# Performance work log

Hardware: AMD Instinct MI355X
Metric: run time of the kernel (lower is better)

## Reference

```python
import jax, jax.numpy as jnp
import numpy as np

TEMPERATURE = 0.07
EPS = 1e-20

B, C, T, N = 16, 128, 8, 1024


def setup_inputs() -> dict:
    key = jax.random.key(0)
    feats = jax.random.normal(key, (B, C, T, N), dtype=jnp.float32)
    return {"feats": feats}


def reference(feats):
    # feats: [B, C, T, N] node features (post encoder+head).
    # L2-normalize along channel dim (FCHead normalizes embeddings in CRW).
    f = feats / (jnp.linalg.norm(feats, axis=1, keepdims=True) + 1e-12)

    # calc_affinity: pairwise affinity between consecutive frames -> [B, T-1, N, N]
    A = jnp.einsum("bctn,bctm->btnm", f[:, :, :-1], f[:, :, 1:])

    # calc_markov: temperature softmax over last dim (edge dropout off / eval)
    right = jax.nn.softmax(A / TEMPERATURE, axis=-1)                  # forward edges
    left = jax.nn.softmax(A.swapaxes(-1, -2) / TEMPERATURE, axis=-1)  # backward edges

    t_len = feats.shape[2]
    losses = []
    for i in range(1, t_len - 1):
        # palindrome walk: right[0..i] then left[i..0], chained BxNxN matmuls
        path = right[:, 0]
        for t in range(1, i + 1):
            path = path @ right[:, t]
        for t in range(i, -1, -1):
            path = path @ left[:, t]
        # cross_entropy(log(path+EPS), arange(N)) averaged over B*N rows
        logp = jax.nn.log_softmax(jnp.log(path + EPS), axis=-1)  # [B, N, N]
        diag = jnp.diagonal(logp, axis1=-2, axis2=-1)            # [B, N]
        losses.append(-jnp.mean(diag))
    return jnp.mean(jnp.stack(losses))
```

## Files before the change

kernel.cpp:

```cpp
#include <hip/hip_runtime.h>

typedef __attribute__((ext_vector_type(4))) float f32x4;
typedef __attribute__((ext_vector_type(8))) short bf16x8;
typedef __attribute__((ext_vector_type(8))) unsigned short ushort8;

#define NB 16
#define NC 128
#define NT 8
#define NN 1024
#define INV_T (1.0f/0.07f)
#define LDW 40

__device__ __forceinline__ unsigned short f2bf(float x){
  union { float f; unsigned int u; } v; v.f = x;
  unsigned int r = v.u + 0x7fffu + ((v.u >> 16) & 1u);
  return (unsigned short)(r >> 16);
}

__device__ __forceinline__ unsigned char f2fp8_sw(float x){
  if(!(x >= 9.765625e-4f)) return 0;
  if(x >= 448.f) return 0x7E;
  union { float f; unsigned int u; } v; v.f = x;
  int e = (int)((v.u >> 23) & 255) - 127;
  if(e >= -6){
    unsigned int m = v.u & 0x7FFFFFu;
    unsigned int r = m + 0x7FFFFu + ((m >> 20) & 1u);
    if(r & 0x800000u){ e++; r = 0; }
    unsigned int b = ((unsigned)(e + 7) << 3) | ((r >> 20) & 7u);
    if(b >= 0x7Fu) b = 0x7Eu;
    return (unsigned char)b;
  } else {
    float t = x * 512.f;
    int q = (int)(t + 0.5f);
    return (unsigned char)q;
  }
}

__device__ __forceinline__ unsigned int pk2fp8(float a, float b){
#if __has_builtin(__builtin_amdgcn_cvt_pk_fp8_f32)
  return (unsigned int)__builtin_amdgcn_cvt_pk_fp8_f32(a, b, 0, false);
#else
  return (unsigned int)f2fp8_sw(a) | ((unsigned int)f2fp8_sw(b) << 8);
#endif
}

__device__ __forceinline__ void gload16(const void* g, void* l){
  __builtin_amdgcn_global_load_lds((const __attribute__((address_space(1))) unsigned int*)g,
                                   (__attribute__((address_space(3))) unsigned int*)l,
                                   16, 0, 0);
}

__global__ void k_norm(const float* __restrict__ feats, unsigned short* __restrict__ fbuf){
  int n = blockIdx.x * 256 + threadIdx.x;
  int b = blockIdx.y >> 3, t = blockIdx.y & 7;
  const float* src = feats + (((size_t)b * NC) * NT + t) * NN + n;
  float ss = 0.f;
  #pragma unroll 8
  for(int c = 0; c < NC; c++){ float v = src[(size_t)c * NT * NN]; ss += v * v; }
  float sc = 1.f / (sqrtf(ss) + 1e-12f);
  unsigned short* dst = fbuf + (((size_t)b * NT + t) * NN + n) * NC;
  #pragma unroll 8
  for(int c = 0; c < NC; c++){ float v = src[(size_t)c * NT * NN]; dst[c] = f2bf(v * sc); }
}

__device__ __forceinline__ void stage_s(const unsigned short* __restrict__ g, int ldg, unsigned short* lds){
  int tid = threadIdx.x;
  #pragma unroll
  for(int j = 0; j < 2; j++){
    int chunk = tid + j * 256;
    int row = chunk >> 2, kc = chunk & 3;
    *(ushort8*)(lds + row * LDW + kc * 8) = *(const ushort8*)(g + (size_t)row * ldg + kc * 8);
  }
}

__device__ __forceinline__ bf16x8 frag_s(const unsigned short* lds, int r0, int lane){
  return *(const bf16x8*)(lds + (r0 + (lane & 15)) * LDW + (lane >> 4) * 8);
}

template<int MODE>
__global__ void gemm_small(const unsigned short* __restrict__ fbuf,
                           unsigned char* __restrict__ G,
                           float* __restrict__ rb, float* __restrict__ cb,
                           unsigned char* __restrict__ P0, unsigned char* __restrict__ M0,
                           int tsel)
{
  __shared__ __align__(16) unsigned short lA[128*LDW];
  __shared__ __align__(16) unsigned short lB[128*LDW];
  int b, t, brow, bcol;
  if(MODE == 0){
    int lin = blockIdx.x, x8 = lin & 7, q = lin >> 3;
    int blk = q & 63, g = (q >> 6) * 8 + x8;
    b = g / 7; t = g % 7;
    brow = (blk >> 3) << 7; bcol = (blk & 7) << 7;
  } else if(MODE == 2){
    int lin = blockIdx.x, x8 = lin & 7, q = lin >> 3;
    int blk = q & 63;
    b = (q >> 6) * 8 + x8; t = 0;
    brow = (blk >> 3) << 7; bcol = (blk & 7) << 7;
  } else {
    b = blockIdx.z; t = tsel;
    brow = blockIdx.x * 128; bcol = blockIdx.y * 128;
  }
  int tA = (MODE==2) ? 0 : t+1;
  int tB = (MODE==2) ? 1 : t;
  const unsigned short* Ab = fbuf + ((size_t)(b*NT+tA)*NN + brow) * NC;
  const unsigned short* Bb = fbuf + ((size_t)(b*NT+tB)*NN + bcol) * NC;
  int tid = threadIdx.x, lane = tid & 63, w = tid >> 6, wr = w >> 1, wc = w & 1;
  f32x4 acc[4][4];
  #pragma unroll
  for(int m=0;m<4;m++)
    #pragma unroll
    for(int n=0;n<4;n++) acc[m][n] = (f32x4){0.f,0.f,0.f,0.f};

  for(int kk=0; kk<4; kk++){
    __syncthreads();
    stage_s(Ab + kk*32, NC, lA);
    stage_s(Bb + kk*32, NC, lB);
    __syncthreads();
    bf16x8 fa[4], fg[4];
    #pragma unroll
    for(int x=0;x<4;x++){ fa[x] = frag_s(lA, wr*64+x*16, lane); fg[x] = frag_s(lB, wc*64+x*16, lane); }
    #pragma unroll
    for(int m=0;m<4;m++)
      #pragma unroll
      for(int n=0;n<4;n++)
        acc[m][n] = __builtin_amdgcn_mfma_f32_16x16x32_bf16(fa[m], fg[n], acc[m][n], 0, 0, 0);
  }

  float e[4][4][4];
  #pragma unroll
  for(int m=0;m<4;m++)
    #pragma unroll
    for(int n=0;n<4;n++)
      #pragma unroll
      for(int j=0;j<4;j++) e[m][n][j] = __expf(acc[m][n][j] * INV_T);

  if(MODE == 0){
    float* cbt = cb + ((size_t)b*7 + t) * NN;
    float* rbt = rb + ((size_t)b*7 + t) * NN;
    #pragma unroll
    for(int m=0;m<4;m++)
      #pragma unroll
      for(int j=0;j<4;j++){
        float s = e[m][0][j]+e[m][1][j]+e[m][2][j]+e[m][3][j];
        s += __shfl_xor(s,1); s += __shfl_xor(s,2); s += __shfl_xor(s,4); s += __shfl_xor(s,8);
        if((lane & 15) == 0){
          int row = brow + wr*64 + m*16 + (lane>>4)*4 + j;
          atomicAdd(&cbt[row], s);
        }
      }
    #pragma unroll
    for(int n=0;n<4;n++){
      float s = 0.f;
      #pragma unroll
      for(int m=0;m<4;m++)
        #pragma unroll
        for(int j=0;j<4;j++) s += e[m][n][j];
      s += __shfl_xor(s,16); s += __shfl_xor(s,32);
      if((lane >> 4) == 0){
        int col = bcol + wc*64 + n*16 + lane;
        atomicAdd(&rbt[col], s);
      }
    }
    if(G && t >= 1){
      unsigned char* Gt = G + ((size_t)(t-1)*NB + b) * ((size_t)NN*NN);
      #pragma unroll
      for(int m=0;m<4;m++)
        #pragma unroll
        for(int j=0;j<4;j++){
          int row = brow + wr*64 + m*16 + (lane>>4)*4 + j;
          unsigned char* gr = Gt + (size_t)row * NN + bcol + wc*64 + (lane&15);
          unsigned int p01 = pk2fp8(e[m][0][j]*0.0625f, e[m][1][j]*0.0625f);
          unsigned int p23 = pk2fp8(e[m][2][j]*0.0625f, e[m][3][j]*0.0625f);
          gr[0]  = (unsigned char)p01;
          gr[16] = (unsigned char)(p01 >> 8);
          gr[32] = (unsigned char)p23;
          gr[48] = (unsigned char)(p23 >> 8);
        }
    }
  } else if(MODE == 1){
    unsigned char* Gt = G + ((size_t)b << 20);
    #pragma unroll
    for(int m=0;m<4;m++)
      #pragma unroll
      for(int j=0;j<4;j++){
        int row = brow + wr*64 + m*16 + (lane>>4)*4 + j;
        unsigned char* gr = Gt + (size_t)row * NN + bcol + wc*64 + (lane&15);
        unsigned int p01 = pk2fp8(e[m][0][j]*0.0625f, e[m][1][j]*0.0625f);
        unsigned int p23 = pk2fp8(e[m][2][j]*0.0625f, e[m][3][j]*0.0625f);
        gr[0]  = (unsigned char)p01;
        gr[16] = (unsigned char)(p01 >> 8);
        gr[32] = (unsigned char)p23;
        gr[48] = (unsigned char)(p23 >> 8);
      }
  } else {
    const float* r0 = rb + (size_t)b*7*NN;
    const float* r1 = r0 + NN;
    const float* c0 = cb + (size_t)b*7*NN;
    unsigned char* Pt = P0 + ((size_t)b << 20);
    unsigned char* Mt = M0 + ((size_t)b << 20);
    float r1i[4], c0i[4];
    #pragma unroll
    for(int n=0;n<4;n++){
      int col = bcol + wc*64 + n*16 + (lane&15);
      r1i[n] = 65536.f / r1[col];
      c0i[n] = 1024.f / c0[col];
    }
    #pragma unroll
    for(int m=0;m<4;m++)
      #pragma unroll
      for(int j=0;j<4;j++){
        int row = brow + wr*64 + m*16 + (lane>>4)*4 + j;
        float r0i = 1.f / r0[row];
        unsigned char* pr = Pt + (size_t)row * NN + bcol + wc*64 + (lane&15);
        unsigned char* mr = Mt + (size_t)row * NN + bcol + wc*64 + (lane&15);
        unsigned int a01 = pk2fp8(e[m][0][j]*r0i*r1i[0], e[m][1][j]*r0i*r1i[1]);
        unsigned int a23 = pk2fp8(e[m][2][j]*r0i*r1i[2], e[m][3][j]*r0i*r1i[3]);
        unsigned int b01 = pk2fp8(e[m][0][j]*c0i[0], e[m][1][j]*c0i[1]);
        unsigned int b23 = pk2fp8(e[m][2][j]*c0i[2], e[m][3][j]*c0i[3]);
        pr[0]  = (unsigned char)a01;  pr[16] = (unsigned char)(a01 >> 8);
        pr[32] = (unsigned char)a23;  pr[48] = (unsigned char)(a23 >> 8);
        mr[0]  = (unsigned char)b01;  mr[16] = (unsigned char)(b01 >> 8);
        mr[32] = (unsigned char)b23;  mr[48] = (unsigned char)(b23 >> 8);
      }
  }
}

template<int LAST>
__global__ void __launch_bounds__(512, 2)
k_chain(const unsigned char* __restrict__ P, const unsigned char* __restrict__ M,
        const unsigned char* __restrict__ G,
        unsigned char* __restrict__ Pn, unsigned char* __restrict__ Mn,
        const float* __restrict__ rb, const float* __restrict__ cb,
        float* __restrict__ diag, int i)
{
  __shared__ __align__(16) unsigned char lP0[128*64], lM0[128*64], lG0[256*64];
  __shared__ __align__(16) unsigned char lP1[128*64], lM1[128*64], lG1[256*64];
  int lin = blockIdx.x, x8 = lin & 7, q = lin >> 3;
  int jj = q & 15, g = (q >> 4) * 8 + x8;
  int b = g >> 1, cbp = g & 1;
  int rowb = jj >> 1, cbk = cbp * 2 + (jj & 1);
  size_t mb = (size_t)b << 20;
  int brow = rowb * 128, bcol = cbk * 256;
  const unsigned char* Pb = P + mb + (size_t)brow * NN;
  const unsigned char* Mb = M + mb + (size_t)brow * NN;
  const unsigned char* Gb = G + mb + (size_t)bcol * NN;
  int tid = threadIdx.x, lane = tid & 63, w = tid >> 6, wr = w >> 2, wc = w & 3;
  int l15 = lane & 15, g4 = lane >> 4, sm = l15 & 6;

  int srow = tid >> 2;
  int gOff = (((tid & 3) ^ ((srow >> 1) & 3)) << 4);
  int so0 = ((g4 ^ sm) << 3);

  f32x4 aP[4][4], aM[4][4];
  #pragma unroll
  for(int m=0;m<4;m++)
    #pragma unroll
    for(int n=0;n<4;n++){ aP[m][n] = (f32x4){0.f,0.f,0.f,0.f}; aM[m][n] = (f32x4){0.f,0.f,0.f,0.f}; }

  auto stage = [&](int kk, unsigned char* lp, unsigned char* lm, unsigned char* lg){
    const unsigned char* ps = Pb + kk*64 + gOff;
    const unsigned char* ms = Mb + kk*64 + gOff;
    const unsigned char* gs = Gb + kk*64 + gOff;
    gload16(ps + (size_t)srow*NN,       lp + tid*16);
    gload16(ms + (size_t)srow*NN,       lm + tid*16);
    gload16(gs + (size_t)srow*NN,       lg + tid*16);
    gload16(gs + (size_t)(srow+128)*NN, lg + 8192 + tid*16);
  };

  auto compute = [&](const unsigned char* lp, const unsigned char* lm, const unsigned char* lg){
    #pragma unroll
    for(int kh = 0; kh < 2; kh++){
      int so = so0 ^ (kh << 5);
      long fP[4], fM[4], fG[4];
      #pragma unroll
      for(int x=0;x<4;x++){
        fP[x] = *(const long*)(lp + (wr*64 + x*16 + l15)*64 + so);
        fM[x] = *(const long*)(lm + (wr*64 + x*16 + l15)*64 + so);
        fG[x] = *(const long*)(lg + (wc*64 + x*16 + l15)*64 + so);
      }
      #pragma unroll
      for(int m=0;m<4;m++)
        #pragma unroll
        for(int n=0;n<4;n++){
          aP[m][n] = __builtin_amdgcn_mfma_f32_16x16x32_fp8_fp8(fP[m], fG[n], aP[m][n], 0, 0, 0);
          aM[m][n] = __builtin_amdgcn_mfma_f32_16x16x32_fp8_fp8(fM[m], fG[n], aM[m][n], 0, 0, 0);
        }
    }
  };

  stage(0, lP0, lM0, lG0);
  __syncthreads();
  #pragma unroll 1
  for(int kk = 0; kk < 16; kk += 2){
    if(kk + 1 < 16) stage(kk+1, lP1, lM1, lG1);
    compute(lP0, lM0, lG0);
    __syncthreads();
    if(kk + 2 < 16) stage(kk+2, lP0, lM0, lG0);
    compute(lP1, lM1, lG1);
    __syncthreads();
  }

  const float* ccur = cb + ((size_t)b*7 + i) * NN;
  const float* rnxt = rb + ((size_t)b*7 + i + 1) * NN;
  float cid[4], ciw[4], ri[4];
  #pragma unroll
  for(int n=0;n<4;n++){
    int col = bcol + wc*64 + n*16 + l15;
    float c1 = 1.f / ccur[col];
    cid[n] = c1;
    ciw[n] = 16.f * c1;
    ri[n]  = LAST ? 0.f : 16.f / rnxt[col];
  }
  float* dg = diag + ((size_t)b*6 + (i-1)) * NN;
  #pragma unroll
  for(int m=0;m<4;m++)
    #pragma unroll
    for(int j4=0;j4<4;j4++){
      int rowi = brow + wr*64 + m*16 + (lane>>4)*4 + j4;
      float s = 0.f;
      #pragma unroll
      for(int n=0;n<4;n++)
        s += aP[m][n][j4] * aM[m][n][j4] * cid[n];
      if(!LAST){
        unsigned char* pr = Pn + mb + (size_t)rowi * NN + bcol + wc*64 + l15;
        unsigned char* mr = Mn + mb + (size_t)rowi * NN + bcol + wc*64 + l15;
        unsigned int a01 = pk2fp8(aP[m][0][j4]*ri[0], aP[m][1][j4]*ri[1]);
        unsigned int a23 = pk2fp8(aP[m][2][j4]*ri[2], aP[m][3][j4]*ri[3]);
        unsigned int b01 = pk2fp8(aM[m][0][j4]*ciw[0], aM[m][1][j4]*ciw[1]);
        unsigned int b23 = pk2fp8(aM[m][2][j4]*ciw[2], aM[m][3][j4]*ciw[3]);
        pr[0]  = (unsigned char)a01;  pr[16] = (unsigned char)(a01 >> 8);
        pr[32] = (unsigned char)a23;  pr[48] = (unsigned char)(a23 >> 8);
        mr[0]  = (unsigned char)b01;  mr[16] = (unsigned char)(b01 >> 8);
        mr[32] = (unsigned char)b23;  mr[48] = (unsigned char)(b23 >> 8);
      }
      s += __shfl_xor(s,1); s += __shfl_xor(s,2); s += __shfl_xor(s,4); s += __shfl_xor(s,8);
      if((lane&15)==0) atomicAdd(&dg[rowi], s * (1.f/262144.f));
    }
}

__global__ void k_loss(const float* __restrict__ diag, float* __restrict__ out){
  __shared__ float red[16];
  float s = 0.f;
  for(int idx = threadIdx.x; idx < NB*6*NN; idx += 1024) s += __logf(diag[idx] + 1e-20f);
  s += __shfl_xor(s,1); s += __shfl_xor(s,2); s += __shfl_xor(s,4);
  s += __shfl_xor(s,8); s += __shfl_xor(s,16); s += __shfl_xor(s,32);
  if((threadIdx.x & 63) == 0) red[threadIdx.x >> 6] = s;
  __syncthreads();
  if(threadIdx.x == 0){
    float t = 0.f;
    for(int k = 0; k < 16; k++) t += red[k];
    out[0] = -t / (6.0f * NB * NN);
  }
}

__global__ void k_fail(float* out){ out[0] = 1.0e9f; }

extern "C" void kernel_launch(void* const* d_in, const int* in_sizes, int n_in,
                              void* d_out, int out_size, void* d_ws, size_t ws_size,
                              hipStream_t stream) {
  const float* feats = (const float*)d_in[0];
  float* out = (float*)d_out;
  char* ws = (char*)d_ws;
  size_t off = 0;
  auto alloc = [&](size_t bytes) -> char* {
    char* p = ws + off; off += (bytes + 255) & ~(size_t)255; return p;
  };
  const size_t plane = (size_t)NB * NN * NN;
  unsigned short* fb = (unsigned short*)alloc((size_t)NB*NT*NN*NC*2);
  unsigned char* Pa   = (unsigned char*)alloc(plane);
  unsigned char* Pbuf = (unsigned char*)alloc(plane);
  unsigned char* Ma   = (unsigned char*)alloc(plane);
  unsigned char* Mbuf = (unsigned char*)alloc(plane);
  float* rb = (float*)alloc((size_t)NB*7*NN*4);
  float* cb = (float*)alloc((size_t)NB*7*NN*4);
  float* dg = (float*)alloc((size_t)NB*6*NN*4);
  if(off + plane > ws_size){ k_fail<<<1,1,0,stream>>>(out); return; }
  bool big = (off + 6*plane) <= ws_size;
  unsigned char* G = (unsigned char*)alloc(big ? 6*plane : plane);

  hipMemsetAsync(rb, 0, (size_t)NB*7*NN*4 + (size_t)NB*7*NN*4 + (size_t)NB*6*NN*4, stream);

  k_norm<<<dim3(4, NB*NT), 256, 0, stream>>>(feats, fb);
  gemm_small<0><<<dim3(7168), 256, 0, stream>>>(fb, big ? G : nullptr, rb, cb, nullptr, nullptr, 0);
  gemm_small<2><<<dim3(1024), 256, 0, stream>>>(fb, nullptr, rb, cb, Pa, Ma, 0);

  unsigned char *Pold = Pa, *Mold = Ma, *Pnew = Pbuf, *Mnew = Mbuf;
  for(int i = 1; i <= 6; i++){
    unsigned char* Gi;
    if(big){
      Gi = G + (size_t)(i-1) * NB * NN * NN;
    } else {
      gemm_small<1><<<dim3(8,8,NB), 256, 0, stream>>>(fb, G, rb, cb, nullptr, nullptr, i);
      Gi = G;
    }
    if(i < 6)
      k_chain<0><<<dim3(512), 512, 0, stream>>>(Pold, Mold, Gi, Pnew, Mnew, rb, cb, dg, i);
    else
      k_chain<1><<<dim3(512), 512, 0, stream>>>(Pold, Mold, Gi, Pnew, Mnew, rb, cb, dg, i);
    unsigned char* tp = Pold; Pold = Pnew; Pnew = tp;
    unsigned char* tm = Mold; Mold = Mnew; Mnew = tm;
  }
  k_loss<<<1, 1024, 0, stream>>>(dg, out);
}
```

Before: 557.1 us.

## Pack fp8 outputs into word stores and use swizzled direct-to-LDS loads

Every kernel that writes fp8 P, M and G tiles now issues one 4-byte store per row fragment instead of four scattered byte stores. This changes the column order inside each 64-wide block, so consumers must agree with the permuted layout. The small affinity GEMM also stages its bf16 operands with global_load_lds into an unpadded LDS tile and uses an XOR swizzle to avoid bank conflicts, replacing register round-trips through padded LDS. The aim is to cut store-instruction count and staging overhead, at the risk of a layout mismatch between producers and consumers.

```diff
diff --git a/kernel.cpp b/kernel.cpp
--- a/kernel.cpp
+++ b/kernel.cpp
@@ -9,7 +9,7 @@
 #define NT 8
 #define NN 1024
 #define INV_T (1.0f/0.07f)
-#define LDW 40
+
 
 __device__ __forceinline__ unsigned short f2bf(float x){
   union { float f; unsigned int u; } v; v.f = x;
@@ -63,20 +63,6 @@
   for(int c = 0; c < NC; c++){ float v = src[(size_t)c * NT * NN]; dst[c] = f2bf(v * sc); }
 }
 
-__device__ __forceinline__ void stage_s(const unsigned short* __restrict__ g, int ldg, unsigned short* lds){
-  int tid = threadIdx.x;
-  #pragma unroll
-  for(int j = 0; j < 2; j++){
-    int chunk = tid + j * 256;
-    int row = chunk >> 2, kc = chunk & 3;
-    *(ushort8*)(lds + row * LDW + kc * 8) = *(const ushort8*)(g + (size_t)row * ldg + kc * 8);
-  }
-}
-
-__device__ __forceinline__ bf16x8 frag_s(const unsigned short* lds, int r0, int lane){
-  return *(const bf16x8*)(lds + (r0 + (lane & 15)) * LDW + (lane >> 4) * 8);
-}
-
 template<int MODE>
 __global__ void gemm_small(const unsigned short* __restrict__ fbuf,
                            unsigned char* __restrict__ G,
@@ -84,8 +70,8 @@
                            unsigned char* __restrict__ P0, unsigned char* __restrict__ M0,
                            int tsel)
 {
-  __shared__ __align__(16) unsigned short lA[128*LDW];
-  __shared__ __align__(16) unsigned short lB[128*LDW];
+  __shared__ __align__(16) unsigned short lA[128*32];
+  __shared__ __align__(16) unsigned short lB[128*32];
   int b, t, brow, bcol;
   if(MODE == 0){
     int lin = blockIdx.x, x8 = lin & 7, q = lin >> 3;
@@ -106,6 +92,9 @@
   const unsigned short* Ab = fbuf + ((size_t)(b*NT+tA)*NN + brow) * NC;
   const unsigned short* Bb = fbuf + ((size_t)(b*NT+tB)*NN + bcol) * NC;
   int tid = threadIdx.x, lane = tid & 63, w = tid >> 6, wr = w >> 1, wc = w & 1;
+  int l15 = lane & 15, g4 = lane >> 4;
+  int rchunk = (g4 ^ ((l15 >> 1) & 3)) << 3;
+
   f32x4 acc[4][4];
   #pragma unroll
   for(int m=0;m<4;m++)
@@ -114,12 +103,21 @@
 
   for(int kk=0; kk<4; kk++){
     __syncthreads();
-    stage_s(Ab + kk*32, NC, lA);
-    stage_s(Bb + kk*32, NC, lB);
+    #pragma unroll
+    for(int j = 0; j < 2; j++){
+      int ch = tid + j*256;
+      int row = ch >> 2, c = ch & 3;
+      int sc = (c ^ ((row >> 1) & 3)) << 3;
+      gload16(Ab + (size_t)row*NC + kk*32 + sc, lA + ch*8);
+      gload16(Bb + (size_t)row*NC + kk*32 + sc, lB + ch*8);
+    }
     __syncthreads();
     bf16x8 fa[4], fg[4];
     #pragma unroll
-    for(int x=0;x<4;x++){ fa[x] = frag_s(lA, wr*64+x*16, lane); fg[x] = frag_s(lB, wc*64+x*16, lane); }
+    for(int x=0;x<4;x++){
+      fa[x] = *(const bf16x8*)(lA + (wr*64 + x*16 + l15)*32 + rchunk);
+      fg[x] = *(const bf16x8*)(lB + (wc*64 + x*16 + l15)*32 + rchunk);
+    }
     #pragma unroll
     for(int m=0;m<4;m++)
       #pragma unroll
@@ -169,13 +167,9 @@
         #pragma unroll
         for(int j=0;j<4;j++){
           int row = brow + wr*64 + m*16 + (lane>>4)*4 + j;
-          unsigned char* gr = Gt + (size_t)row * NN + bcol + wc*64 + (lane&15);
           unsigned int p01 = pk2fp8(e[m][0][j]*0.0625f, e[m][1][j]*0.0625f);
           unsigned int p23 = pk2fp8(e[m][2][j]*0.0625f, e[m][3][j]*0.0625f);
-          gr[0]  = (unsigned char)p01;
-          gr[16] = (unsigned char)(p01 >> 8);
-          gr[32] = (unsigned char)p23;
-          gr[48] = (unsigned char)(p23 >> 8);
+          *(unsigned int*)(Gt + (size_t)row * NN + bcol + wc*64 + l15*4) = p01 | (p23 << 16);
         }
     }
   } else if(MODE == 1){
@@ -185,13 +179,9 @@
       #pragma unroll
       for(int j=0;j<4;j++){
         int row = brow + wr*64 + m*16 + (lane>>4)*4 + j;
-        unsigned char* gr = Gt + (size_t)row * NN + bcol + wc*64 + (lane&15);
         unsigned int p01 = pk2fp8(e[m][0][j]*0.0625f, e[m][1][j]*0.0625f);
         unsigned int p23 = pk2fp8(e[m][2][j]*0.0625f, e[m][3][j]*0.0625f);
-        gr[0]  = (unsigned char)p01;
-        gr[16] = (unsigned char)(p01 >> 8);
-        gr[32] = (unsigned char)p23;
-        gr[48] = (unsigned char)(p23 >> 8);
+        *(unsigned int*)(Gt + (size_t)row * NN + bcol + wc*64 + l15*4) = p01 | (p23 << 16);
       }
   } else {
     const float* r0 = rb + (size_t)b*7*NN;
@@ -202,7 +192,7 @@
     float r1i[4], c0i[4];
     #pragma unroll
     for(int n=0;n<4;n++){
-      int col = bcol + wc*64 + n*16 + (lane&15);
+      int col = bcol + wc*64 + n*16 + l15;
       r1i[n] = 65536.f / r1[col];
       c0i[n] = 1024.f / c0[col];
     }
@@ -212,16 +202,12 @@
       for(int j=0;j<4;j++){
         int row = brow + wr*64 + m*16 + (lane>>4)*4 + j;
         float r0i = 1.f / r0[row];
-        unsigned char* pr = Pt + (size_t)row * NN + bcol + wc*64 + (lane&15);
-        unsigned char* mr = Mt + (size_t)row * NN + bcol + wc*64 + (lane&15);
         unsigned int a01 = pk2fp8(e[m][0][j]*r0i*r1i[0], e[m][1][j]*r0i*r1i[1]);
         unsigned int a23 = pk2fp8(e[m][2][j]*r0i*r1i[2], e[m][3][j]*r0i*r1i[3]);
         unsigned int b01 = pk2fp8(e[m][0][j]*c0i[0], e[m][1][j]*c0i[1]);
         unsigned int b23 = pk2fp8(e[m][2][j]*c0i[2], e[m][3][j]*c0i[3]);
-        pr[0]  = (unsigned char)a01;  pr[16] = (unsigned char)(a01 >> 8);
-        pr[32] = (unsigned char)a23;  pr[48] = (unsigned char)(a23 >> 8);
-        mr[0]  = (unsigned char)b01;  mr[16] = (unsigned char)(b01 >> 8);
-        mr[32] = (unsigned char)b23;  mr[48] = (unsigned char)(b23 >> 8);
+        *(unsigned int*)(Pt + (size_t)row * NN + bcol + wc*64 + l15*4) = a01 | (a23 << 16);
+        *(unsigned int*)(Mt + (size_t)row * NN + bcol + wc*64 + l15*4) = b01 | (b23 << 16);
       }
   }
 }
@@ -323,16 +309,12 @@
       for(int n=0;n<4;n++)
         s += aP[m][n][j4] * aM[m][n][j4] * cid[n];
       if(!LAST){
-        unsigned char* pr = Pn + mb + (size_t)rowi * NN + bcol + wc*64 + l15;
-        unsigned char* mr = Mn + mb + (size_t)rowi * NN + bcol + wc*64 + l15;
         unsigned int a01 = pk2fp8(aP[m][0][j4]*ri[0], aP[m][1][j4]*ri[1]);
         unsigned int a23 = pk2fp8(aP[m][2][j4]*ri[2], aP[m][3][j4]*ri[3]);
         unsigned int b01 = pk2fp8(aM[m][0][j4]*ciw[0], aM[m][1][j4]*ciw[1]);
         unsigned int b23 = pk2fp8(aM[m][2][j4]*ciw[2], aM[m][3][j4]*ciw[3]);
-        pr[0]  = (unsigned char)a01;  pr[16] = (unsigned char)(a01 >> 8);
-        pr[32] = (unsigned char)a23;  pr[48] = (unsigned char)(a23 >> 8);
-        mr[0]  = (unsigned char)b01;  mr[16] = (unsigned char)(b01 >> 8);
-        mr[32] = (unsigned char)b23;  mr[48] = (unsigned char)(b23 >> 8);
+        *(unsigned int*)(Pn + mb + (size_t)rowi * NN + bcol + wc*64 + l15*4) = a01 | (a23 << 16);
+        *(unsigned int*)(Mn + mb + (size_t)rowi * NN + bcol + wc*64 + l15*4) = b01 | (b23 << 16);
       }
       s += __shfl_xor(s,1); s += __shfl_xor(s,2); s += __shfl_xor(s,4); s += __shfl_xor(s,8);
       if((lane&15)==0) atomicAdd(&dg[rowi], s * (1.f/262144.f));
```

Measured after the change: 501.0 us. 1.11x faster.
